# Kernel optimization log

Measured on AMD Instinct MI355X. Metric: run time of the kernel, lower is better.

## Reference

```python
import jax, jax.numpy as jnp
import numpy as np

T, H, E, I, K = 2048, 2048, 8, 5632, 2

def setup_inputs() -> dict:
    key = jax.random.key(0)
    k1, k2, k3, k4, k5 = jax.random.split(key, 5)
    scale_w = 1.0 / np.sqrt(H)
    return {
        "hidden_states": jax.random.normal(k1, (T, H), dtype=jnp.float32),
        "w13": jax.random.normal(k2, (E, 2 * I, H), dtype=jnp.float32) * scale_w,
        "w2": jax.random.normal(k3, (E, H, I), dtype=jnp.float32) * (1.0 / np.sqrt(I)),
        "topk_weights": jax.random.uniform(k4, (T, K), dtype=jnp.float32),
        "topk_ids": jax.random.randint(k5, (T, K), 0, E, dtype=jnp.int64 if jax.config.jax_enable_x64 else jnp.int32),
    }

def reference(hidden_states, w13, w2, topk_weights, topk_ids):
    # hidden_states: [T,H]; w13: [E,2I,H]; w2: [E,H,I]; topk_*: [T,K]
    E_, twoI, _ = w13.shape
    I_ = twoI // 2
    # grouped GEMM 1: all experts' gate/up projections  -> [E,T,2I]
    h13 = jnp.einsum('th,enh->etn', hidden_states, w13)
    g1 = h13[..., :I_]          # w1 (gate) half, matches torch.chunk dim=0
    g3 = h13[..., I_:]          # w3 (up) half
    act = jax.nn.silu(g1) * g3  # [E,T,I]
    # grouped GEMM 2: down projection -> [E,T,H]
    expert_out = jnp.einsum('eti,ehi->eth', act, w2)
    # routing combine; source applies expert_id % 4 (replicated faithfully)
    eid = topk_ids % 4                                   # [T,K]
    comb = jax.nn.one_hot(eid, E_, dtype=hidden_states.dtype) * topk_weights[..., None]  # [T,K,E]
    route = comb.sum(axis=1).T                           # [E,T]
    out = jnp.einsum('eth,et->th', expert_out, route)    # [T,H]
    return out
```

## Files before the change

### kernel.cpp

```cpp
#include <hip/hip_runtime.h>

typedef float f32x4 __attribute__((ext_vector_type(4)));
typedef __bf16 bf16x8 __attribute__((ext_vector_type(8)));
typedef unsigned short u16;
typedef u16 u16x4 __attribute__((ext_vector_type(4)));


__device__ __forceinline__ u16 f2bf(float x) {
  union { float f; unsigned int u; } v; v.f = x;
  unsigned int u = v.u;
  return (u16)((u + 0x7FFFu + ((u >> 16) & 1u)) >> 16);
}

__device__ __forceinline__ void gld_lds16(const void* g, void* l) {
  __builtin_amdgcn_global_load_lds((const __attribute__((address_space(1))) void*)g,
                                   (__attribute__((address_space(3))) void*)l,
                                   16, 0, 0);
}


__global__ __launch_bounds__(256) void route_kernel(const int* __restrict__ ids,
                                                    const float* __restrict__ wts,
                                                    float* __restrict__ route4,
                                                    int T, int K) {
  int t = blockIdx.x * 256 + threadIdx.x;
  if (t >= T) return;
  float r[4] = {0.f, 0.f, 0.f, 0.f};
  for (int k = 0; k < K; ++k) {
    int e = ids[t * K + k] & 3;
    r[e] += wts[t * K + k];
  }
#pragma unroll
  for (int e = 0; e < 4; ++e) route4[e * T + t] = r[e];
}

__global__ __launch_bounds__(256) void cvt_bf16(const float* __restrict__ src,
                                                u16* __restrict__ dst, long n) {
  long i = ((long)blockIdx.x * 256 + threadIdx.x) * 4;
  if (i < n) {
    float4 f = *(const float4*)(src + i);
    u16x4 o;
    o.x = f2bf(f.x); o.y = f2bf(f.y); o.z = f2bf(f.z); o.w = f2bf(f.w);
    *(u16x4*)(dst + i) = o;
  }
}

__global__ __launch_bounds__(256, 2) void gemm1_act(const u16* __restrict__ A,
                                                    const u16* __restrict__ Wall,
                                                    const float* __restrict__ route4,
                                                    u16* __restrict__ actall,
                                                    int T, int H, int I) {
  __shared__ __align__(16) u16 sA[128 * 64];
  __shared__ __align__(16) u16 sB[128 * 64];
  const int e = blockIdx.z;
  const u16* W = Wall + (size_t)e * 2 * I * H;
  u16* act = actall + (size_t)e * T * I;
  const int tid = threadIdx.x;
  const int lane = tid & 63;
  const int wm = (tid >> 6) >> 1;
  const int wn = (tid >> 6) & 1;
  const int m0 = blockIdx.y * 128;
  const int n0 = blockIdx.x * 64;

  f32x4 acc1[4][2] = {};
  f32x4 acc3[4][2] = {};

  for (int k0 = 0; k0 < H; k0 += 64) {
    __syncthreads();
#pragma unroll
    for (int q = 0; q < 4; ++q) {
      int l = q * 256 + tid;
      int row = l >> 3;
      int cb = (l & 7) * 8;
      gld_lds16(A + (size_t)(m0 + row) * H + k0 + cb, &sA[l * 8]);
    }
#pragma unroll
    for (int q = 0; q < 4; ++q) {
      int l = q * 256 + tid;
      int row = l >> 3;
      int cb = (l & 7) * 8;
      int grow = (row < 64) ? (n0 + row) : (I + n0 + (row - 64));
      gld_lds16(W + (size_t)grow * H + k0 + cb, &sB[l * 8]);
    }
    __syncthreads();
#pragma unroll
    for (int kk = 0; kk < 64; kk += 32) {
      const int ko = kk + (lane >> 4) * 8;
      bf16x8 af[4];
#pragma unroll
      for (int mi = 0; mi < 4; ++mi)
        af[mi] = *(const bf16x8*)&sA[(wm * 64 + mi * 16 + (lane & 15)) * 64 + ko];
      bf16x8 b1[2], b3[2];
#pragma unroll
      for (int ni = 0; ni < 2; ++ni) {
        int r = wn * 32 + ni * 16 + (lane & 15);
        b1[ni] = *(const bf16x8*)&sB[r * 64 + ko];
        b3[ni] = *(const bf16x8*)&sB[(64 + r) * 64 + ko];
      }
#pragma unroll
      for (int mi = 0; mi < 4; ++mi)
#pragma unroll
        for (int ni = 0; ni < 2; ++ni) {
          acc1[mi][ni] = __builtin_amdgcn_mfma_f32_16x16x32_bf16(af[mi], b1[ni], acc1[mi][ni], 0, 0, 0);
          acc3[mi][ni] = __builtin_amdgcn_mfma_f32_16x16x32_bf16(af[mi], b3[ni], acc3[mi][ni], 0, 0, 0);
        }
    }
  }
  const int col = lane & 15;
  const int r0 = (lane >> 4) * 4;
#pragma unroll
  for (int mi = 0; mi < 4; ++mi)
#pragma unroll
    for (int r = 0; r < 4; ++r) {
      int t = m0 + wm * 64 + mi * 16 + r0 + r;
      float rt = route4[e * T + t];
#pragma unroll
      for (int ni = 0; ni < 2; ++ni) {
        float c1 = acc1[mi][ni][r];
        float c3 = acc3[mi][ni][r];
        float v = rt * (c1 / (1.f + __expf(-c1)) * c3);
        int i = n0 + wn * 32 + ni * 16 + col;
        act[(size_t)t * I + i] = f2bf(v);
      }
    }
}

__global__ __launch_bounds__(256, 2) void gemm2_out(const u16* __restrict__ Aall,
                                                    const u16* __restrict__ W2all,
                                                    float* __restrict__ out,
                                                    int T, int I, int H) {
  __shared__ __align__(16) u16 sA[128 * 64];
  __shared__ __align__(16) u16 sB[128 * 64];
  const int e = blockIdx.z;
  const u16* A = Aall + (size_t)e * T * I;
  const u16* W2 = W2all + (size_t)e * H * I;
  const int tid = threadIdx.x;
  const int lane = tid & 63;
  const int wm = (tid >> 6) >> 1;
  const int wn = (tid >> 6) & 1;
  const int m0 = blockIdx.y * 128;
  const int n0 = blockIdx.x * 128;

  f32x4 acc[4][4] = {};

  for (int k0 = 0; k0 < I; k0 += 64) {
    __syncthreads();
#pragma unroll
    for (int q = 0; q < 4; ++q) {
      int l = q * 256 + tid;
      int row = l >> 3;
      int cb = (l & 7) * 8;
      gld_lds16(A + (size_t)(m0 + row) * I + k0 + cb, &sA[l * 8]);
    }
#pragma unroll
    for (int q = 0; q < 4; ++q) {
      int l = q * 256 + tid;
      int row = l >> 3;
      int cb = (l & 7) * 8;
      gld_lds16(W2 + (size_t)(n0 + row) * I + k0 + cb, &sB[l * 8]);
    }
    __syncthreads();
#pragma unroll
    for (int kk = 0; kk < 64; kk += 32) {
      const int ko = kk + (lane >> 4) * 8;
      bf16x8 af[4], bfr[4];
#pragma unroll
      for (int mi = 0; mi < 4; ++mi)
        af[mi] = *(const bf16x8*)&sA[(wm * 64 + mi * 16 + (lane & 15)) * 64 + ko];
#pragma unroll
      for (int ni = 0; ni < 4; ++ni)
        bfr[ni] = *(const bf16x8*)&sB[(wn * 64 + ni * 16 + (lane & 15)) * 64 + ko];
#pragma unroll
      for (int mi = 0; mi < 4; ++mi)
#pragma unroll
        for (int ni = 0; ni < 4; ++ni)
          acc[mi][ni] = __builtin_amdgcn_mfma_f32_16x16x32_bf16(af[mi], bfr[ni], acc[mi][ni], 0, 0, 0);
    }
  }
  const int col = lane & 15;
  const int r0 = (lane >> 4) * 4;
#pragma unroll
  for (int mi = 0; mi < 4; ++mi)
#pragma unroll
    for (int r = 0; r < 4; ++r) {
      int t = m0 + wm * 64 + mi * 16 + r0 + r;
#pragma unroll
      for (int ni = 0; ni < 4; ++ni) {
        int h = n0 + wn * 64 + ni * 16 + col;
        unsafeAtomicAdd(&out[(size_t)t * H + h], acc[mi][ni][r]);
      }
    }
}


extern "C" void kernel_launch(void* const* d_in, const int* in_sizes, int n_in,
                              void* d_out, int out_size, void* d_ws, size_t ws_size,
                              hipStream_t stream) {
  constexpr int T = 2048, H = 2048, I = 5632, K = 2;
  const float* hidden = (const float*)d_in[0];
  const float* w13 = (const float*)d_in[1];
  const float* w2 = (const float*)d_in[2];
  const float* tw = (const float*)d_in[3];
  const int* tids = (const int*)d_in[4];
  float* out = (float*)d_out;

  const size_t OFF_HB = 32768;
  const size_t OFF_W13 = OFF_HB + (size_t)T * H * 2;
  const size_t OFF_W2 = OFF_W13 + (size_t)4 * 2 * I * H * 2;
  const size_t OFF_ACT = OFF_W2 + (size_t)4 * H * I * 2;
  const size_t WS_NEED = OFF_ACT + (size_t)4 * T * I * 2;
  if (ws_size < WS_NEED) return;

  char* ws = (char*)d_ws;
  float* route4 = (float*)ws;
  u16* hb = (u16*)(ws + OFF_HB);
  u16* w13b = (u16*)(ws + OFF_W13);
  u16* w2b = (u16*)(ws + OFF_W2);
  u16* actb = (u16*)(ws + OFF_ACT);

  route_kernel<<<(T + 255) / 256, 256, 0, stream>>>(tids, tw, route4, T, K);

  const long nh = (long)T * H;
  cvt_bf16<<<(int)((nh / 4 + 255) / 256), 256, 0, stream>>>(hidden, hb, nh);
  const long nw13 = (long)4 * 2 * I * H;
  cvt_bf16<<<(int)((nw13 / 4 + 255) / 256), 256, 0, stream>>>(w13, w13b, nw13);
  const long nw2 = (long)4 * H * I;
  cvt_bf16<<<(int)((nw2 / 4 + 255) / 256), 256, 0, stream>>>(w2, w2b, nw2);

  hipMemsetAsync(out, 0, (size_t)out_size * 4, stream);

  dim3 g1(I / 64, T / 128, 4);
  gemm1_act<<<g1, 256, 0, stream>>>(hb, w13b, route4, actb, T, H, I);

  dim3 g2(H / 128, T / 128, 4);
  gemm2_out<<<g2, 256, 0, stream>>>(actb, w2b, out, T, I, H);
}
```

Baseline: 1.808 ms.

## Swizzle LDS tiles, raise occupancy, replace atomics with per-expert partials plus combine

Applies an XOR swizzle to the 16-byte chunk positions in the shared-memory A/B tiles of both GEMMs to avoid LDS bank conflicts on the MFMA fragment reads. Raises the launch-bounds minimum blocks per SM from 2 to 4. Replaces the float atomic accumulation into the output with plain stores of per-expert partial results into a workspace buffer, followed by a combine kernel that sums the four partials. This removes the memset and the atomic contention but adds extra workspace traffic and another kernel launch.

```diff
diff --git a/kernel.cpp b/kernel.cpp
--- a/kernel.cpp
+++ b/kernel.cpp
@@ -17,6 +17,7 @@
                                    (__attribute__((address_space(3))) void*)l,
                                    16, 0, 0);
 }
+
 
 
 __global__ __launch_bounds__(256) void route_kernel(const int* __restrict__ ids,
@@ -45,7 +46,19 @@
   }
 }
 
-__global__ __launch_bounds__(256, 2) void gemm1_act(const u16* __restrict__ A,
+__global__ __launch_bounds__(256) void combine4(const float* __restrict__ part,
+                                                float* __restrict__ out, long n) {
+  long i = ((long)blockIdx.x * 256 + threadIdx.x) * 4;
+  if (i < n) {
+    f32x4 a = *(const f32x4*)(part + i);
+    f32x4 b = *(const f32x4*)(part + n + i);
+    f32x4 c = *(const f32x4*)(part + 2 * n + i);
+    f32x4 d = *(const f32x4*)(part + 3 * n + i);
+    *(f32x4*)(out + i) = (a + b) + (c + d);
+  }
+}
+
+__global__ __launch_bounds__(256, 4) void gemm1_act(const u16* __restrict__ A,
                                                     const u16* __restrict__ Wall,
                                                     const float* __restrict__ route4,
                                                     u16* __restrict__ actall,
@@ -71,31 +84,32 @@
     for (int q = 0; q < 4; ++q) {
       int l = q * 256 + tid;
       int row = l >> 3;
-      int cb = (l & 7) * 8;
-      gld_lds16(A + (size_t)(m0 + row) * H + k0 + cb, &sA[l * 8]);
-    }
-#pragma unroll
-    for (int q = 0; q < 4; ++q) {
-      int l = q * 256 + tid;
-      int row = l >> 3;
-      int cb = (l & 7) * 8;
+      int gg = (l ^ (l >> 3)) & 7;
+      gld_lds16(A + (size_t)(m0 + row) * H + k0 + gg * 8, &sA[l * 8]);
+    }
+#pragma unroll
+    for (int q = 0; q < 4; ++q) {
+      int l = q * 256 + tid;
+      int row = l >> 3;
+      int gg = (l ^ (l >> 3)) & 7;
       int grow = (row < 64) ? (n0 + row) : (I + n0 + (row - 64));
-      gld_lds16(W + (size_t)grow * H + k0 + cb, &sB[l * 8]);
+      gld_lds16(W + (size_t)grow * H + k0 + gg * 8, &sB[l * 8]);
     }
     __syncthreads();
 #pragma unroll
     for (int kk = 0; kk < 64; kk += 32) {
-      const int ko = kk + (lane >> 4) * 8;
+      const int gbase = (kk >> 3) + (lane >> 4);
+      const int swzo = ((gbase ^ (lane & 7)) << 3);
       bf16x8 af[4];
 #pragma unroll
       for (int mi = 0; mi < 4; ++mi)
-        af[mi] = *(const bf16x8*)&sA[(wm * 64 + mi * 16 + (lane & 15)) * 64 + ko];
+        af[mi] = *(const bf16x8*)&sA[(wm * 64 + mi * 16 + (lane & 15)) * 64 + swzo];
       bf16x8 b1[2], b3[2];
 #pragma unroll
       for (int ni = 0; ni < 2; ++ni) {
         int r = wn * 32 + ni * 16 + (lane & 15);
-        b1[ni] = *(const bf16x8*)&sB[r * 64 + ko];
-        b3[ni] = *(const bf16x8*)&sB[(64 + r) * 64 + ko];
+        b1[ni] = *(const bf16x8*)&sB[r * 64 + swzo];
+        b3[ni] = *(const bf16x8*)&sB[(64 + r) * 64 + swzo];
       }
 #pragma unroll
       for (int mi = 0; mi < 4; ++mi)
@@ -125,15 +139,16 @@
     }
 }
 
-__global__ __launch_bounds__(256, 2) void gemm2_out(const u16* __restrict__ Aall,
-                                                    const u16* __restrict__ W2all,
-                                                    float* __restrict__ out,
-                                                    int T, int I, int H) {
+__global__ __launch_bounds__(256, 4) void gemm2_part(const u16* __restrict__ Aall,
+                                                     const u16* __restrict__ W2all,
+                                                     float* __restrict__ part,
+                                                     int T, int I, int H) {
   __shared__ __align__(16) u16 sA[128 * 64];
   __shared__ __align__(16) u16 sB[128 * 64];
   const int e = blockIdx.z;
   const u16* A = Aall + (size_t)e * T * I;
   const u16* W2 = W2all + (size_t)e * H * I;
+  float* myout = part + (size_t)e * T * H;
   const int tid = threadIdx.x;
   const int lane = tid & 63;
   const int wm = (tid >> 6) >> 1;
@@ -149,27 +164,28 @@
     for (int q = 0; q < 4; ++q) {
       int l = q * 256 + tid;
       int row = l >> 3;
-      int cb = (l & 7) * 8;
-      gld_lds16(A + (size_t)(m0 + row) * I + k0 + cb, &sA[l * 8]);
-    }
-#pragma unroll
-    for (int q = 0; q < 4; ++q) {
-      int l = q * 256 + tid;
-      int row = l >> 3;
-      int cb = (l & 7) * 8;
-      gld_lds16(W2 + (size_t)(n0 + row) * I + k0 + cb, &sB[l * 8]);
+      int gg = (l ^ (l >> 3)) & 7;
+      gld_lds16(A + (size_t)(m0 + row) * I + k0 + gg * 8, &sA[l * 8]);
+    }
+#pragma unroll
+    for (int q = 0; q < 4; ++q) {
+      int l = q * 256 + tid;
+      int row = l >> 3;
+      int gg = (l ^ (l >> 3)) & 7;
+      gld_lds16(W2 + (size_t)(n0 + row) * I + k0 + gg * 8, &sB[l * 8]);
     }
     __syncthreads();
 #pragma unroll
     for (int kk = 0; kk < 64; kk += 32) {
-      const int ko = kk + (lane >> 4) * 8;
+      const int gbase = (kk >> 3) + (lane >> 4);
+      const int swzo = ((gbase ^ (lane & 7)) << 3);
       bf16x8 af[4], bfr[4];
 #pragma unroll
       for (int mi = 0; mi < 4; ++mi)
-        af[mi] = *(const bf16x8*)&sA[(wm * 64 + mi * 16 + (lane & 15)) * 64 + ko];
+        af[mi] = *(const bf16x8*)&sA[(wm * 64 + mi * 16 + (lane & 15)) * 64 + swzo];
 #pragma unroll
       for (int ni = 0; ni < 4; ++ni)
-        bfr[ni] = *(const bf16x8*)&sB[(wn * 64 + ni * 16 + (lane & 15)) * 64 + ko];
+        bfr[ni] = *(const bf16x8*)&sB[(wn * 64 + ni * 16 + (lane & 15)) * 64 + swzo];
 #pragma unroll
       for (int mi = 0; mi < 4; ++mi)
 #pragma unroll
@@ -187,7 +203,7 @@
 #pragma unroll
       for (int ni = 0; ni < 4; ++ni) {
         int h = n0 + wn * 64 + ni * 16 + col;
-        unsafeAtomicAdd(&out[(size_t)t * H + h], acc[mi][ni][r]);
+        myout[(size_t)t * H + h] = acc[mi][ni][r];
       }
     }
 }
@@ -208,7 +224,8 @@
   const size_t OFF_W13 = OFF_HB + (size_t)T * H * 2;
   const size_t OFF_W2 = OFF_W13 + (size_t)4 * 2 * I * H * 2;
   const size_t OFF_ACT = OFF_W2 + (size_t)4 * H * I * 2;
-  const size_t WS_NEED = OFF_ACT + (size_t)4 * T * I * 2;
+  const size_t OFF_PART = OFF_ACT + (size_t)4 * T * I * 2;
+  const size_t WS_NEED = OFF_PART + (size_t)4 * T * H * 4;
   if (ws_size < WS_NEED) return;
 
   char* ws = (char*)d_ws;
@@ -217,6 +234,7 @@
   u16* w13b = (u16*)(ws + OFF_W13);
   u16* w2b = (u16*)(ws + OFF_W2);
   u16* actb = (u16*)(ws + OFF_ACT);
+  float* partb = (float*)(ws + OFF_PART);
 
   route_kernel<<<(T + 255) / 256, 256, 0, stream>>>(tids, tw, route4, T, K);
 
@@ -227,11 +245,12 @@
   const long nw2 = (long)4 * H * I;
   cvt_bf16<<<(int)((nw2 / 4 + 255) / 256), 256, 0, stream>>>(w2, w2b, nw2);
 
-  hipMemsetAsync(out, 0, (size_t)out_size * 4, stream);
-
   dim3 g1(I / 64, T / 128, 4);
   gemm1_act<<<g1, 256, 0, stream>>>(hb, w13b, route4, actb, T, H, I);
 
   dim3 g2(H / 128, T / 128, 4);
-  gemm2_out<<<g2, 256, 0, stream>>>(actb, w2b, out, T, I, H);
-}
+  gemm2_part<<<g2, 256, 0, stream>>>(actb, w2b, partb, T, I, H);
+
+  const long nout = (long)T * H;
+  combine4<<<(int)((nout / 4 + 255) / 256), 256, 0, stream>>>(partb, out, nout);
+}
```

After: 1.609 ms. -11.0%, faster.
